# Performance work log

Hardware: AMD Instinct MI355X
Metric: run time of the kernel (lower is better)

Reference implementation:

```python
import jax, jax.numpy as jnp
import numpy as np

N_NODES = 100000
N_EDGES = 2400000


def setup_inputs() -> dict:
    key = jax.random.key(0)
    ks = jax.random.split(key, 6)
    x = jax.random.normal(ks[0], (N_NODES, 2), dtype=jnp.float32)
    edge_index = jax.random.randint(ks[1], (2, N_EDGES), 0, N_NODES, dtype=jnp.int64)
    # GCNConv weights (glorot-ish scale) and zero biases
    W1 = jax.random.normal(ks[2], (2, 32), dtype=jnp.float32) * (1.0 / np.sqrt(2.0))
    b1 = jnp.zeros((32,), dtype=jnp.float32)
    W2 = jax.random.normal(ks[3], (32, 32), dtype=jnp.float32) * (1.0 / np.sqrt(32.0))
    b2 = jnp.zeros((32,), dtype=jnp.float32)
    W3 = jax.random.normal(ks[4], (32, 1), dtype=jnp.float32) * (1.0 / np.sqrt(32.0))
    b3 = jnp.zeros((1,), dtype=jnp.float32)
    return {"x": x, "edge_index": edge_index, "W1": W1, "b1": b1,
            "W2": W2, "b2": b2, "W3": W3, "b3": b3}


def reference(x, edge_index, W1, b1, W2, b2, W3, b3):
    N = x.shape[0]
    self_loops = jnp.arange(N, dtype=edge_index.dtype)
    src = jnp.concatenate([edge_index[0], self_loops])  # message sources
    dst = jnp.concatenate([edge_index[1], self_loops])  # aggregation targets
    # Symmetric GCN normalization: deg computed at target nodes (PyG gcn_norm)
    deg = jax.ops.segment_sum(jnp.ones_like(dst, dtype=x.dtype), dst, num_segments=N)
    dinv = jnp.where(deg > 0, jax.lax.rsqrt(deg), 0.0)
    norm = (dinv[src] * dinv[dst])[:, None]  # [E+N, 1]

    def gcn_layer(h, W, b):
        h = h @ W                                  # [N, out]
        msg = norm * h[src]                        # gather + scale
        agg = jax.ops.segment_sum(msg, dst, num_segments=N)  # scatter-add
        return agg + b

    h = jax.nn.relu(gcn_layer(x, W1, b1))
    h = jax.nn.relu(gcn_layer(h, W2, b2))
    out = gcn_layer(h, W3, b3)
    return out.reshape(-1)
```

## Files before the change

### kernel.cpp

```cpp
#include <hip/hip_runtime.h>

#define NN 100000
#define NE 2400000
#define NB 391
#define CAP 6912
#define EPB 2048

__device__ __forceinline__ int wexscan(int v, int lane) {
    int x = v;
#pragma unroll
    for (int off = 1; off < 64; off <<= 1) {
        int t = __shfl_up(x, off, 64);
        x += (lane >= off) ? t : 0;
    }
    return x - v;
}

__global__ __launch_bounds__(512) void k_binscatter(const int* __restrict__ ei,
        int* __restrict__ cur, int* __restrict__ binned) {
    __shared__ int hist[NB], lbase[NB], myb[NB];
    __shared__ int stage[EPB];
    __shared__ unsigned short stageb[EPB];
    __shared__ int wsum[8];
    int tid = threadIdx.x;
    for (int i = tid; i < NB; i += 512) hist[i] = 0;
    __syncthreads();
    int base_e = blockIdx.x * EPB + tid * 4;
    int pk[4], bn[4], rk[4];
    if (base_e + 4 <= NE) {
        int4 sa = *(const int4*)(ei + base_e);
        int4 da = *(const int4*)(ei + NE + base_e);
        int ss[4] = {sa.x, sa.y, sa.z, sa.w};
        int dd[4] = {da.x, da.y, da.z, da.w};
#pragma unroll
        for (int k = 0; k < 4; ++k) {
            bn[k] = dd[k] >> 8;
            pk[k] = ss[k] | ((dd[k] & 255) << 17);
            rk[k] = atomicAdd(&hist[bn[k]], 1);
        }
    } else {
#pragma unroll
        for (int k = 0; k < 4; ++k) bn[k] = -1;
    }
    __syncthreads();
    int lane = tid & 63, wid = tid >> 6;
    int v = (tid < NB) ? hist[tid] : 0;
    int ex = wexscan(v, lane);
    if (lane == 63) wsum[wid] = ex + v;
    __syncthreads();
    int woff = 0, tot = 0;
#pragma unroll
    for (int i = 0; i < 8; ++i) {
        int s = wsum[i];
        woff += (i < wid) ? s : 0;
        tot += s;
    }
    ex += woff;
    if (tid < NB) {
        lbase[tid] = ex;
        if (v > 0) myb[tid] = tid * CAP + atomicAdd(&cur[tid], v);
    }
    __syncthreads();
#pragma unroll
    for (int k = 0; k < 4; ++k) {
        if (bn[k] >= 0) {
            int slot = lbase[bn[k]] + rk[k];
            stage[slot] = pk[k];
            stageb[slot] = (unsigned short)bn[k];
        }
    }
    __syncthreads();
    for (int j = tid; j < tot; j += 512) {
        int b = stageb[j];
        binned[myb[b] + (j - lbase[b])] = stage[j];
    }
}

__global__ __launch_bounds__(256) void k_csr_count(const int* __restrict__ binned,
        const int* __restrict__ cur, const float* __restrict__ x,
        int* __restrict__ rsp, float* __restrict__ dinv, float2* __restrict__ xs) {
    __shared__ int cnt[256];
    __shared__ int wsum[4];
    int tid = threadIdx.x, b = blockIdx.x;
    int base = b * CAP, n = cur[b];
    cnt[tid] = 0;
    __syncthreads();
    int n4 = n >> 2;
    const int4* b4 = (const int4*)(binned + base);
    for (int j = tid; j < n4; j += 256) {
        int4 w = b4[j];
        atomicAdd(&cnt[(w.x >> 17) & 255], 1);
        atomicAdd(&cnt[(w.y >> 17) & 255], 1);
        atomicAdd(&cnt[(w.z >> 17) & 255], 1);
        atomicAdd(&cnt[(w.w >> 17) & 255], 1);
    }
    for (int j = (n4 << 2) + tid; j < n; j += 256)
        atomicAdd(&cnt[(binned[base + j] >> 17) & 255], 1);
    __syncthreads();
    int deg = cnt[tid];
    int lane = tid & 63, wid = tid >> 6;
    int ex = wexscan(deg, lane);
    if (lane == 63) wsum[wid] = ex + deg;
    __syncthreads();
    int woff = 0;
#pragma unroll
    for (int i = 0; i < 4; ++i) woff += (i < wid) ? wsum[i] : 0;
    ex += woff;
    int node = (b << 8) + tid;
    if (node < NN) {
        rsp[node] = ((base + ex) << 8) | deg;
        float di = rsqrtf((float)(deg + 1));
        dinv[node] = di;
        float2 xv = ((const float2*)x)[node];
        xs[node] = make_float2(di * xv.x, di * xv.y);
    }
}

__global__ __launch_bounds__(256) void k_csr_place(const int* __restrict__ binned,
        const int* __restrict__ cur, const int* __restrict__ rsp,
        const float2* __restrict__ xs, const float* __restrict__ dinv,
        int* __restrict__ csr, float4* __restrict__ At) {
    __shared__ int cur2[256];
    int tid = threadIdx.x, b = blockIdx.x;
    int base = b * CAP, n = cur[b];
    int node = (b << 8) + tid;
    int rp = (node < NN) ? rsp[node] : 0;
    cur2[tid] = (node < NN) ? ((rp >> 8) - base) : 0;
    __syncthreads();
    int n4 = n >> 2;
    const int4* b4 = (const int4*)(binned + base);
    for (int j = tid; j < n4; j += 256) {
        int4 w = b4[j];
        int p0 = atomicAdd(&cur2[(w.x >> 17) & 255], 1); csr[base + p0] = w.x & 0x1FFFF;
        int p1 = atomicAdd(&cur2[(w.y >> 17) & 255], 1); csr[base + p1] = w.y & 0x1FFFF;
        int p2 = atomicAdd(&cur2[(w.z >> 17) & 255], 1); csr[base + p2] = w.z & 0x1FFFF;
        int p3 = atomicAdd(&cur2[(w.w >> 17) & 255], 1); csr[base + p3] = w.w & 0x1FFFF;
    }
    for (int j = (n4 << 2) + tid; j < n; j += 256) {
        int w = binned[base + j];
        int p = atomicAdd(&cur2[(w >> 17) & 255], 1);
        csr[base + p] = w & 0x1FFFF;
    }
    __syncthreads();
    if (node < NN) {
        int beg = rp >> 8, deg = rp & 255;
        float ax = 0.f, ay = 0.f;
        int e = beg, end = beg + deg;
        for (; e + 4 <= end; e += 4) {
            int s0 = csr[e], s1 = csr[e + 1], s2 = csr[e + 2], s3 = csr[e + 3];
            float2 v0 = xs[s0], v1 = xs[s1], v2 = xs[s2], v3 = xs[s3];
            ax += (v0.x + v1.x) + (v2.x + v3.x);
            ay += (v0.y + v1.y) + (v2.y + v3.y);
        }
        for (; e < end; ++e) { float2 vv = xs[csr[e]]; ax += vv.x; ay += vv.y; }
        float di = dinv[node];
        float2 xn = xs[node];
        At[node] = make_float4(di * (ax + xn.x), di * (ay + xn.y), di, 0.f);
    }
}

__global__ __launch_bounds__(256) void k_gather_fly(const float4* __restrict__ At,
        const int* __restrict__ rsp, const int* __restrict__ csr,
        const float* __restrict__ W1, const float* __restrict__ b1,
        const float* __restrict__ W2, const float* __restrict__ b2,
        const float* __restrict__ W3, float* __restrict__ h3) {
    __shared__ float WsT[32 * 36];
    __shared__ float accS[256];
    __shared__ float4 stage[8][32];
    int tid = threadIdx.x;
    for (int j = tid; j < 1024; j += 256) {
        int k = j >> 5, fo = j & 31;
        WsT[fo * 36 + k] = W2[j];
    }
    __syncthreads();
    int g = tid >> 5, f = tid & 31;
    int node = blockIdx.x * 8 + g;
    float w0f = W1[f], w1f = W1[32 + f], bf = b1[f];
    float4 an = At[node];
    int r = rsp[node];
    float di = an.z;
    float vs = fmaf(an.y, w1f, fmaf(an.x, w0f, bf));
    float acc0 = di * fmaxf(vs, 0.f), acc1 = 0.f;
    int beg = r >> 8, deg = r & 255;
    float4* st = &stage[g][0];
    for (int b0 = 0; b0 < deg; b0 += 32) {
        float4 a = make_float4(0.f, 0.f, 0.f, 0.f);
        if (b0 + f < deg) a = At[csr[beg + b0 + f]];
        st[f] = a;
        __asm__ __volatile__("" ::: "memory");
#pragma unroll
        for (int j = 0; j < 32; j += 2) {
            float4 e0 = st[j], e1 = st[j + 1];
            float v0 = fmaf(e0.y, w1f, fmaf(e0.x, w0f, bf));
            acc0 = fmaf(e0.z, fmaxf(v0, 0.f), acc0);
            float v1 = fmaf(e1.y, w1f, fmaf(e1.x, w0f, bf));
            acc1 = fmaf(e1.z, fmaxf(v1, 0.f), acc1);
        }
        __asm__ __volatile__("" ::: "memory");
    }
    accS[tid] = di * (acc0 + acc1);
    __asm__ __volatile__("" ::: "memory");
    int n0 = tid & 224;
    float sum = b2[f];
    const float* wrow = &WsT[f * 36];
#pragma unroll
    for (int k = 0; k < 32; k += 4) {
        float4 a4 = *(const float4*)&accS[n0 + k];
        float4 w4 = *(const float4*)&wrow[k];
        sum = fmaf(a4.x, w4.x, sum);
        sum = fmaf(a4.y, w4.y, sum);
        sum = fmaf(a4.z, w4.z, sum);
        sum = fmaf(a4.w, w4.w, sum);
    }
    float h2 = fmaxf(sum, 0.f);
    float v = di * h2 * W3[f];
#pragma unroll
    for (int off = 16; off > 0; off >>= 1) v += __shfl_down(v, off, 32);
    if (f == 0) h3[node] = v;
}

__global__ __launch_bounds__(256) void k_gather_out(const float* __restrict__ hs,
        const int* __restrict__ rsp, const int* __restrict__ csr,
        const float* __restrict__ dinv, const float* __restrict__ bias,
        float* __restrict__ out) {
    int node = blockIdx.x * 256 + threadIdx.x;
    if (node >= NN) return;
    int r = rsp[node];
    int beg = r >> 8, end = beg + (r & 255);
    float acc = hs[node];
    int e = beg;
    for (; e + 4 <= end; e += 4) {
        int s0 = csr[e], s1 = csr[e + 1], s2 = csr[e + 2], s3 = csr[e + 3];
        acc += (hs[s0] + hs[s1]) + (hs[s2] + hs[s3]);
    }
    for (; e < end; ++e) acc += hs[csr[e]];
    out[node] = dinv[node] * acc + bias[0];
}

extern "C" void kernel_launch(void* const* d_in, const int* in_sizes, int n_in,
                              void* d_out, int out_size, void* d_ws, size_t ws_size,
                              hipStream_t stream) {
    const float* x  = (const float*)d_in[0];
    const int*   ei = (const int*)d_in[1];
    const float* W1 = (const float*)d_in[2];
    const float* b1 = (const float*)d_in[3];
    const float* W2 = (const float*)d_in[4];
    const float* b2 = (const float*)d_in[5];
    const float* W3 = (const float*)d_in[6];
    const float* b3 = (const float*)d_in[7];
    float* out = (float*)d_out;

    char* w = (char*)d_ws;
    float4* At    = (float4*)w; w += NN * 16;
    float2* xs    = (float2*)w; w += NN * 8;
    int*   cur    = (int*)w;    w += NB * 4;
    int*   rsp    = (int*)w;    w += NN * 4;
    float* dinv   = (float*)w;  w += NN * 4;
    int*   binned = (int*)w;    w += NB * CAP * 4;
    int*   csr    = (int*)w;    w += NB * CAP * 4;
    float* h3     = (float*)w;  w += NN * 4;

    const int G_BS  = (NE + EPB - 1) / EPB;
    const int G_N   = (NN + 255) / 256;
    const int G_G   = NN / 8;

    hipMemsetAsync(cur, 0, NB * 4, stream);
    k_binscatter<<<G_BS, 512, 0, stream>>>(ei, cur, binned);
    k_csr_count<<<NB, 256, 0, stream>>>(binned, cur, x, rsp, dinv, xs);
    k_csr_place<<<NB, 256, 0, stream>>>(binned, cur, rsp, xs, dinv, csr, At);
    k_gather_fly<<<G_G, 256, 0, stream>>>(At, rsp, csr, W1, b1, W2, b2, W3, h3);
    k_gather_out<<<G_N, 256, 0, stream>>>(h3, rsp, csr, dinv, b3, out);
}
```

Baseline: 199.4 us.

## Replace global atomic bin reservation with per-block histogram plus offset scan

```diff
diff --git a/kernel.cpp b/kernel.cpp
--- a/kernel.cpp
+++ b/kernel.cpp
@@ -4,7 +4,8 @@
 #define NE 2400000
 #define NB 391
 #define CAP 6912
-#define EPB 2048
+#define EPB 4096
+#define NBLK2 ((NE + EPB - 1) / EPB)
 
 __device__ __forceinline__ int wexscan(int v, int lane) {
     int x = v;
@@ -16,31 +17,80 @@
     return x - v;
 }
 
-__global__ __launch_bounds__(512) void k_binscatter(const int* __restrict__ ei,
-        int* __restrict__ cur, int* __restrict__ binned) {
+__global__ __launch_bounds__(512) void k_hist(const int* __restrict__ ei,
+        int* __restrict__ bh) {
+    __shared__ int hist[NB];
+    int tid = threadIdx.x;
+    for (int i = tid; i < NB; i += 512) hist[i] = 0;
+    __syncthreads();
+    int base_e = blockIdx.x * EPB + tid * 8;
+    if (base_e + 8 <= NE) {
+        int4 da = *(const int4*)(ei + NE + base_e);
+        int4 db = *(const int4*)(ei + NE + base_e + 4);
+        atomicAdd(&hist[da.x >> 8], 1); atomicAdd(&hist[da.y >> 8], 1);
+        atomicAdd(&hist[da.z >> 8], 1); atomicAdd(&hist[da.w >> 8], 1);
+        atomicAdd(&hist[db.x >> 8], 1); atomicAdd(&hist[db.y >> 8], 1);
+        atomicAdd(&hist[db.z >> 8], 1); atomicAdd(&hist[db.w >> 8], 1);
+    }
+    __syncthreads();
+    for (int i = tid; i < NB; i += 512) bh[blockIdx.x * NB + i] = hist[i];
+}
+
+__global__ __launch_bounds__(256) void k_offscan(int* __restrict__ bh,
+        int* __restrict__ tot) {
+    __shared__ int wsum[4];
+    int b = blockIdx.x, tid = threadIdx.x;
+    int lane = tid & 63, wid = tid >> 6;
+    int carry = 0;
+#pragma unroll
+    for (int r = 0; r < 3; ++r) {
+        int blk = r * 256 + tid;
+        int v = (blk < NBLK2) ? bh[blk * NB + b] : 0;
+        int ex = wexscan(v, lane);
+        if (lane == 63) wsum[wid] = ex + v;
+        __syncthreads();
+        int woff = 0, rt = 0;
+#pragma unroll
+        for (int i = 0; i < 4; ++i) {
+            woff += (i < wid) ? wsum[i] : 0;
+            rt += wsum[i];
+        }
+        if (blk < NBLK2) bh[blk * NB + b] = b * CAP + carry + woff + ex;
+        carry += rt;
+        __syncthreads();
+    }
+    if (tid == 0) tot[b] = carry;
+}
+
+__global__ __launch_bounds__(512) void k_scatter2(const int* __restrict__ ei,
+        const int* __restrict__ bh, int* __restrict__ binned) {
     __shared__ int hist[NB], lbase[NB], myb[NB];
     __shared__ int stage[EPB];
     __shared__ unsigned short stageb[EPB];
     __shared__ int wsum[8];
     int tid = threadIdx.x;
-    for (int i = tid; i < NB; i += 512) hist[i] = 0;
-    __syncthreads();
-    int base_e = blockIdx.x * EPB + tid * 4;
-    int pk[4], bn[4], rk[4];
-    if (base_e + 4 <= NE) {
-        int4 sa = *(const int4*)(ei + base_e);
-        int4 da = *(const int4*)(ei + NE + base_e);
-        int ss[4] = {sa.x, sa.y, sa.z, sa.w};
-        int dd[4] = {da.x, da.y, da.z, da.w};
-#pragma unroll
-        for (int k = 0; k < 4; ++k) {
+    for (int i = tid; i < NB; i += 512) {
+        hist[i] = 0;
+        myb[i] = bh[blockIdx.x * NB + i];
+    }
+    __syncthreads();
+    int base_e = blockIdx.x * EPB + tid * 8;
+    int pk[8], bn[8], rk[8];
+    if (base_e + 8 <= NE) {
+        const int4* s4 = (const int4*)(ei + base_e);
+        const int4* d4 = (const int4*)(ei + NE + base_e);
+        int4 sa = s4[0], sb = s4[1], da = d4[0], db = d4[1];
+        int ss[8] = {sa.x, sa.y, sa.z, sa.w, sb.x, sb.y, sb.z, sb.w};
+        int dd[8] = {da.x, da.y, da.z, da.w, db.x, db.y, db.z, db.w};
+#pragma unroll
+        for (int k = 0; k < 8; ++k) {
             bn[k] = dd[k] >> 8;
             pk[k] = ss[k] | ((dd[k] & 255) << 17);
             rk[k] = atomicAdd(&hist[bn[k]], 1);
         }
     } else {
 #pragma unroll
-        for (int k = 0; k < 4; ++k) bn[k] = -1;
+        for (int k = 0; k < 8; ++k) bn[k] = -1;
     }
     __syncthreads();
     int lane = tid & 63, wid = tid >> 6;
@@ -56,13 +106,10 @@
         tot += s;
     }
     ex += woff;
-    if (tid < NB) {
-        lbase[tid] = ex;
-        if (v > 0) myb[tid] = tid * CAP + atomicAdd(&cur[tid], v);
-    }
-    __syncthreads();
-#pragma unroll
-    for (int k = 0; k < 4; ++k) {
+    if (tid < NB) lbase[tid] = ex;
+    __syncthreads();
+#pragma unroll
+    for (int k = 0; k < 8; ++k) {
         if (bn[k] >= 0) {
             int slot = lbase[bn[k]] + rk[k];
             stage[slot] = pk[k];
@@ -77,12 +124,12 @@
 }
 
 __global__ __launch_bounds__(256) void k_csr_count(const int* __restrict__ binned,
-        const int* __restrict__ cur, const float* __restrict__ x,
+        const int* __restrict__ tot, const float* __restrict__ x,
         int* __restrict__ rsp, float* __restrict__ dinv, float2* __restrict__ xs) {
     __shared__ int cnt[256];
     __shared__ int wsum[4];
     int tid = threadIdx.x, b = blockIdx.x;
-    int base = b * CAP, n = cur[b];
+    int base = b * CAP, n = tot[b];
     cnt[tid] = 0;
     __syncthreads();
     int n4 = n >> 2;
@@ -117,12 +164,12 @@
 }
 
 __global__ __launch_bounds__(256) void k_csr_place(const int* __restrict__ binned,
-        const int* __restrict__ cur, const int* __restrict__ rsp,
+        const int* __restrict__ tot, const int* __restrict__ rsp,
         const float2* __restrict__ xs, const float* __restrict__ dinv,
         int* __restrict__ csr, float4* __restrict__ At) {
     __shared__ int cur2[256];
     int tid = threadIdx.x, b = blockIdx.x;
-    int base = b * CAP, n = cur[b];
+    int base = b * CAP, n = tot[b];
     int node = (b << 8) + tid;
     int rp = (node < NN) ? rsp[node] : 0;
     cur2[tid] = (node < NN) ? ((rp >> 8) - base) : 0;
@@ -253,21 +300,22 @@
     char* w = (char*)d_ws;
     float4* At    = (float4*)w; w += NN * 16;
     float2* xs    = (float2*)w; w += NN * 8;
-    int*   cur    = (int*)w;    w += NB * 4;
+    int*   bh     = (int*)w;    w += NBLK2 * NB * 4;
+    int*   tot    = (int*)w;    w += NB * 4;
     int*   rsp    = (int*)w;    w += NN * 4;
     float* dinv   = (float*)w;  w += NN * 4;
     int*   binned = (int*)w;    w += NB * CAP * 4;
     int*   csr    = (int*)w;    w += NB * CAP * 4;
     float* h3     = (float*)w;  w += NN * 4;
 
-    const int G_BS  = (NE + EPB - 1) / EPB;
-    const int G_N   = (NN + 255) / 256;
-    const int G_G   = NN / 8;
-
-    hipMemsetAsync(cur, 0, NB * 4, stream);
-    k_binscatter<<<G_BS, 512, 0, stream>>>(ei, cur, binned);
-    k_csr_count<<<NB, 256, 0, stream>>>(binned, cur, x, rsp, dinv, xs);
-    k_csr_place<<<NB, 256, 0, stream>>>(binned, cur, rsp, xs, dinv, csr, At);
+    const int G_N = (NN + 255) / 256;
+    const int G_G = NN / 8;
+
+    k_hist<<<NBLK2, 512, 0, stream>>>(ei, bh);
+    k_offscan<<<NB, 256, 0, stream>>>(bh, tot);
+    k_scatter2<<<NBLK2, 512, 0, stream>>>(ei, bh, binned);
+    k_csr_count<<<NB, 256, 0, stream>>>(binned, tot, x, rsp, dinv, xs);
+    k_csr_place<<<NB, 256, 0, stream>>>(binned, tot, rsp, xs, dinv, csr, At);
     k_gather_fly<<<G_G, 256, 0, stream>>>(At, rsp, csr, W1, b1, W2, b2, W3, h3);
     k_gather_out<<<G_N, 256, 0, stream>>>(h3, rsp, csr, dinv, b3, out);
 }
```

After: 188.4 us. 5.5% less time.
